# Kernel tuning notes

Hardware: AMD Instinct MI355X
Metric: run time of the kernel (lower is better)

Reference implementation:

```python
import jax, jax.numpy as jnp
import numpy as np

MARGIN = 0.5
EPS = 1e-5
NOISE_RATE = 0.5


def setup_inputs() -> dict:
    key = jax.random.key(0)
    k1, k2, k3, k4, k5 = jax.random.split(key, 5)
    n, m, d, c = 1024, 65536, 512, 10000
    return {
        "inputs_col": jax.random.normal(k1, (n, d), dtype=jnp.float32),
        "inputs_row": jax.random.normal(k2, (m, d), dtype=jnp.float32),
        "center": jax.random.normal(k3, (c, d), dtype=jnp.float32),
        "targets_col": jax.random.randint(k4, (n,), 0, c, dtype=jnp.int64),
        "target_row": jax.random.randint(k5, (m,), 0, c, dtype=jnp.int64),
        "filled_mask": jnp.ones((c,), dtype=bool),
    }


def _prism_keep(features, targets, center, filled_mask, noise_rate):
    # no_grad in the original -> stop_gradient here
    f = jax.lax.stop_gradient(features)
    c = jax.lax.stop_gradient(center)
    # all_sim_exp[cls] / sum(all_sim_exp) is exactly softmax over class logits
    probs = jax.nn.softmax(f @ c.T, axis=-1)          # [n, num_classes]
    sel = jnp.take_along_axis(probs, targets[:, None], axis=1)[:, 0]  # [n]
    C = jnp.where(filled_mask[targets], sel, 1.0)      # not-in-memory -> 1
    n = C.shape[0]
    n_remove = int(noise_rate * n)                     # static
    to_remove = jnp.argsort(C)[:n_remove]
    # empty margin_window path: keep everything except to_remove
    keep = jnp.ones((n,), dtype=bool).at[to_remove].set(False)
    return keep


def reference(inputs_col, inputs_row, center, targets_col, target_row, filled_mask):
    n = inputs_col.shape[0]
    sim = inputs_col @ inputs_row.T                    # [n, m]
    pos_mask = targets_col[:, None] == target_row[None, :]
    neg_mask = (~pos_mask) & (sim > MARGIN)
    pos_mask = pos_mask & (sim < 1.0 - EPS)

    keep = _prism_keep(inputs_col, targets_col, center, filled_mask, NOISE_RATE)
    pos_mask = pos_mask & keep[:, None]
    neg_mask = neg_mask & keep[:, None]

    # sum over selected pairs without boolean-indexing (masked reductions)
    pos_loss = jnp.sum(jnp.where(pos_mask, 1.0 - sim, 0.0))
    neg_loss = jnp.sum(jnp.where(neg_mask, sim, 0.0))
    loss = (pos_loss + neg_loss) / n
    return loss, keep
```

## Files before the change

kernel.cpp:

```cpp
#include <hip/hip_runtime.h>


typedef int    v4i   __attribute__((ext_vector_type(4)));
typedef float  f32x4 __attribute__((ext_vector_type(4)));
typedef unsigned char u8;

#define N_COL  1024
#define M_ROW  65536
#define DDIM   512
#define NCLS   10000
#define NT     79
#define NREM   512

#define OFF_A8   0u
#define OFF_C8   524288u
#define OFF_PMS  39256064u
#define OFF_LT   39903232u
#define OFF_COMP 39907328u
#define OFF_TCC  39909376u
#define OFF_ACC  39911424u
#define OFF_CNT  39911432u

__device__ __forceinline__ void async16(const void* g, void* l) {
    __builtin_amdgcn_global_load_lds(
        (const __attribute__((address_space(1))) void*)g,
        (__attribute__((address_space(3))) void*)l, 16, 0, 0);
}

__device__ __forceinline__ unsigned pack4_fp8(float4 v) {
    int r = 0;
    r = __builtin_amdgcn_cvt_pk_fp8_f32(v.x, v.y, r, false);
    r = __builtin_amdgcn_cvt_pk_fp8_f32(v.z, v.w, r, true);
    return (unsigned)r;
}

__device__ __forceinline__ void gemm8_128(const u8* __restrict__ A,
                                          const u8* __restrict__ B,
                                          int m0, int n0,
                                          u8* As, u8* Bs, f32x4 (&acc)[4][4]) {
    const int tid = threadIdx.x, wid = tid >> 6, lane = tid & 63;
    const int wm = wid >> 1, wn = wid & 1;
    const int q = lane >> 4, lc = lane & 15;

    const u8* gA[4]; const u8* gB[4]; int voff[4];
#pragma unroll
    for (int s = 0; s < 4; ++s) {
        const int c  = wid * 256 + s * 64 + lane;
        const int r  = c >> 3;
        const int gs = (c & 7) ^ (r & 7);
        gA[s] = A + (size_t)(m0 + r) * DDIM + gs * 16;
        gB[s] = B + (size_t)(n0 + r) * DDIM + gs * 16;
        voff[s] = c * 16;
    }
#pragma unroll
    for (int i = 0; i < 4; ++i)
#pragma unroll
        for (int j = 0; j < 4; ++j) acc[i][j] = (f32x4){0.f, 0.f, 0.f, 0.f};

    for (int kt = 0; kt < 4; ++kt) {
        const int kb = kt * 128;
#pragma unroll
        for (int s = 0; s < 4; ++s) {
            async16(gA[s] + kb, As + voff[s]);
            async16(gB[s] + kb, Bs + voff[s]);
        }
        __syncthreads();
#pragma unroll
        for (int ks = 0; ks < 4; ++ks) {
            const int gg = ks * 2 + (q >> 1);
            const int bo = (q & 1) * 8;
            long long af[4], bv[4];
#pragma unroll
            for (int i = 0; i < 4; ++i) {
                const int rA = wm * 64 + i * 16 + lc;
                af[i] = *(const long long*)(As + (rA * 8 + (gg ^ (rA & 7))) * 16 + bo);
                const int rB = wn * 64 + i * 16 + lc;
                bv[i] = *(const long long*)(Bs + (rB * 8 + (gg ^ (rB & 7))) * 16 + bo);
            }
#pragma unroll
            for (int i = 0; i < 4; ++i)
#pragma unroll
                for (int j = 0; j < 4; ++j)
                    acc[i][j] = __builtin_amdgcn_mfma_f32_16x16x32_fp8_fp8(
                        af[i], bv[j], acc[i][j], 0, 0, 0);
        }
        __syncthreads();
    }
}

__global__ void k_prep(const float4* __restrict__ a4, const float4* __restrict__ c4,
                       const float* __restrict__ a32, const float* __restrict__ c32,
                       const int* __restrict__ tcol,
                       unsigned* __restrict__ A8w, uint2* __restrict__ C8w,
                       float* __restrict__ lt, double* __restrict__ accd,
                       unsigned* __restrict__ cnt) {
    const int b = blockIdx.x, tid = threadIdx.x;
    if (b == 0 && tid == 0) { *accd = 0.0; *cnt = 0u; }
    if (b < 256) {
        const int idx = b * 256 + tid;
        A8w[idx * 2]     = pack4_fp8(a4[idx * 2]);
        A8w[idx * 2 + 1] = pack4_fp8(a4[idx * 2 + 1]);
    } else if (b < 2784) {
        const int cidx = (b - 256) * 256 + tid;
        const int row  = cidx >> 6;
        uint2 o = make_uint2(0u, 0u);
        if (row < NCLS) {
            o.x = pack4_fp8(c4[cidx * 2]);
            o.y = pack4_fp8(c4[cidx * 2 + 1]);
        }
        C8w[cidx] = o;
    } else {
        const int w = (b - 2784) * 4 + (tid >> 6), lane = tid & 63;
        const int t = tcol[w];
        const float* ar = a32 + (size_t)w * DDIM;
        const float* cr = c32 + (size_t)t * DDIM;
        float s = 0.f;
#pragma unroll
        for (int k = 0; k < DDIM / 64; ++k) s += ar[lane + k * 64] * cr[lane + k * 64];
        for (int off = 32; off; off >>= 1) s += __shfl_down(s, off, 64);
        if (lane == 0) lt[w] = s;
    }
}

__global__ __launch_bounds__(256, 3) void k_mid(const u8* __restrict__ A8,
                                                const u8* __restrict__ C8,
                                                float2* __restrict__ pms) {
    const int b = blockIdx.x, tid = threadIdx.x;
    __shared__ __align__(16) u8 As[16384], Bs[16384];
    __shared__ float s_mm[128][2], s_ss[128][2];
    const int n_t = b >> 3, m0 = (b & 7) * 128, n0 = n_t * 128;
    f32x4 acc[4][4];
    gemm8_128(A8, C8, m0, n0, As, Bs, acc);

    const int wid = tid >> 6, lane = tid & 63;
    const int wm = wid >> 1, wn = wid & 1, q = lane >> 4, lc = lane & 15;
    const int cbase = n0 + wn * 64 + lc;
#pragma unroll
    for (int i = 0; i < 4; ++i) {
#pragma unroll
        for (int reg = 0; reg < 4; ++reg) {
            float mm = -INFINITY, ss = 0.f;
#pragma unroll
            for (int j = 0; j < 4; ++j)
                if (cbase + j * 16 < NCLS) mm = fmaxf(mm, acc[i][j][reg]);
#pragma unroll
            for (int j = 0; j < 4; ++j)
                if (cbase + j * 16 < NCLS) ss += __expf(acc[i][j][reg] - mm);
#pragma unroll
            for (int d2 = 1; d2 < 16; d2 <<= 1) {
                float mo = __shfl_xor(mm, d2, 16);
                float so = __shfl_xor(ss, d2, 16);
                float M = fmaxf(mm, mo), S = 0.f;
                if (ss > 0.f) S += ss * __expf(mm - M);
                if (so > 0.f) S += so * __expf(mo - M);
                mm = M; ss = S;
            }
            if (lc == 0) {
                const int row = i * 16 + q * 4 + reg;
                s_mm[wm * 64 + row][wn] = mm;
                s_ss[wm * 64 + row][wn] = ss;
            }
        }
    }
    __syncthreads();
    if (tid < 128) {
        float m1 = s_mm[tid][0], s1 = s_ss[tid][0];
        float m2 = s_mm[tid][1], s2 = s_ss[tid][1];
        float M = fmaxf(m1, m2), S = 0.f;
        if (s1 > 0.f) S += s1 * __expf(m1 - M);
        if (s2 > 0.f) S += s2 * __expf(m2 - M);
        pms[(size_t)n_t * N_COL + m0 + tid] = make_float2(M, S);
    }
}

__global__ __launch_bounds__(1024) void k_sel(const float2* __restrict__ pms,
                                              const float* __restrict__ lt,
                                              const int* __restrict__ tcol,
                                              int* __restrict__ comp,
                                              int* __restrict__ tcc,
                                              float* __restrict__ keep_out) {
    __shared__ float v[N_COL];
    const int i = threadIdx.x;
    float M = -INFINITY, S = 0.f;
    for (int t = 0; t < NT; ++t) {
        float2 p = pms[(size_t)t * N_COL + i];
        if (p.y > 0.f) {
            if (p.x > M) { S = S * __expf(M - p.x) + p.y; M = p.x; }
            else         { S += p.y * __expf(p.x - M); }
        }
    }
    const float x = lt[i] - (M + logf(S));
    v[i] = x;
    __syncthreads();
    int rank = 0;
    const float4* v4 = (const float4*)v;
#pragma unroll 8
    for (int j4 = 0; j4 < N_COL / 4; ++j4) {
        float4 w = v4[j4];
        const int j = j4 * 4;
        rank += (w.x < x) || (w.x == x && j     < i);
        rank += (w.y < x) || (w.y == x && j + 1 < i);
        rank += (w.z < x) || (w.z == x && j + 2 < i);
        rank += (w.w < x) || (w.w == x && j + 3 < i);
    }
    const bool keep = rank >= NREM;
    keep_out[i] = keep ? 1.0f : 0.0f;
    if (keep) { comp[rank - NREM] = i; tcc[rank - NREM] = tcol[i]; }
}

__global__ __launch_bounds__(512, 2) void k_loss(const u8* __restrict__ A8,
                                                 const float4* __restrict__ brow4,
                                                 const int* __restrict__ comp,
                                                 const int* __restrict__ tcc,
                                                 const int* __restrict__ trow,
                                                 double* __restrict__ accd,
                                                 unsigned* __restrict__ cnt,
                                                 float* __restrict__ out) {
    __shared__ __align__(16) u8 As[3][32768];
    __shared__ __align__(16) u8 Bs[2][8192];
    __shared__ int s_map[512], s_tc[512], s_tr[128];
    __shared__ float s_red[8];
    const int b = blockIdx.x, tid = threadIdx.x;
    const int n0 = b * 128;
    s_map[tid] = comp[tid];
    s_tc[tid]  = tcc[tid];
    if (tid < 128) s_tr[tid] = trow[n0 + tid];
    __syncthreads();

    const int wid = tid >> 6, lane = tid & 63;
    const int wm = wid >> 1, wn = wid & 1;
    const int q = lane >> 4, lc = lane & 15;

    const u8* gA[4]; int vA[4];
#pragma unroll
    for (int s = 0; s < 4; ++s) {
        const int cc = s * 512 + tid;
        const int r  = cc >> 2, gpos = cc & 3;
        const int g  = gpos ^ ((r >> 1) & 3);
        gA[s] = A8 + (size_t)s_map[r] * DDIM + g * 16;
        vA[s] = cc * 16;
    }
    const int rB0 = tid >> 2, gB0 = tid & 3;
    const float4* gB = brow4 + (size_t)(n0 + rB0) * (DDIM / 4) + gB0 * 4;
    const int vB = (rB0 * 4 + (gB0 ^ ((rB0 >> 1) & 3))) * 16;

    f32x4 acc[8][4];
#pragma unroll
    for (int i = 0; i < 8; ++i)
#pragma unroll
        for (int j = 0; j < 4; ++j) acc[i][j] = (f32x4){0.f, 0.f, 0.f, 0.f};

    auto compute = [&](const u8* Asc, const u8* Bsc) {
#pragma unroll
        for (int ks = 0; ks < 2; ++ks) {
            const int gg = ks * 2 + (q >> 1);
            const int bo = (q & 1) * 8;
            long long af[8], bv[4];
#pragma unroll
            for (int i = 0; i < 8; ++i) {
                const int rA = wm * 128 + i * 16 + lc;
                af[i] = *(const long long*)(Asc + (rA * 4 + (gg ^ ((rA >> 1) & 3))) * 16 + bo);
            }
#pragma unroll
            for (int j = 0; j < 4; ++j) {
                const int rB = wn * 64 + j * 16 + lc;
                bv[j] = *(const long long*)(Bsc + (rB * 4 + (gg ^ ((rB >> 1) & 3))) * 16 + bo);
            }
#pragma unroll
            for (int i = 0; i < 8; ++i)
#pragma unroll
                for (int j = 0; j < 4; ++j)
                    acc[i][j] = __builtin_amdgcn_mfma_f32_16x16x32_fp8_fp8(
                        af[i], bv[j], acc[i][j], 0, 0, 0);
        }
    };

    float4 fb[2][4];

#pragma unroll
    for (int s = 0; s < 4; ++s) async16(gA[s], As[0] + vA[s]);
#pragma unroll
    for (int g = 0; g < 4; ++g) fb[0][g] = gB[g];
    __builtin_amdgcn_sched_barrier(0);
#pragma unroll
    for (int s = 0; s < 4; ++s) async16(gA[s] + 64, As[1] + vA[s]);
#pragma unroll
    for (int g = 0; g < 4; ++g) fb[1][g] = gB[16 + g];
    asm volatile("s_waitcnt vmcnt(8)" ::: "memory");
    __builtin_amdgcn_sched_barrier(0);
    {
        uint4 pk;
        pk.x = pack4_fp8(fb[0][0]); pk.y = pack4_fp8(fb[0][1]);
        pk.z = pack4_fp8(fb[0][2]); pk.w = pack4_fp8(fb[0][3]);
        *(uint4*)(Bs[0] + vB) = pk;
    }
    asm volatile("s_waitcnt lgkmcnt(0)" ::: "memory");
    __builtin_amdgcn_s_barrier();

#pragma unroll
    for (int kt = 0; kt < 8; ++kt) {
        if (kt < 6) {
            const int kb = (kt + 2) * 64;
#pragma unroll
            for (int s = 0; s < 4; ++s) async16(gA[s] + kb, As[(kt + 2) % 3] + vA[s]);
#pragma unroll
            for (int g = 0; g < 4; ++g) fb[kt & 1][g] = gB[(kt + 2) * 16 + g];
            asm volatile("s_waitcnt vmcnt(8)" ::: "memory");
        } else if (kt == 6) {
            asm volatile("s_waitcnt vmcnt(0)" ::: "memory");
        }
        __builtin_amdgcn_sched_barrier(0);
        if (kt < 7) {
            uint4 pk;
            pk.x = pack4_fp8(fb[(kt + 1) & 1][0]); pk.y = pack4_fp8(fb[(kt + 1) & 1][1]);
            pk.z = pack4_fp8(fb[(kt + 1) & 1][2]); pk.w = pack4_fp8(fb[(kt + 1) & 1][3]);
            *(uint4*)(Bs[(kt + 1) & 1] + vB) = pk;
        }
        compute(As[kt % 3], Bs[kt & 1]);
        if (kt < 7) {
            asm volatile("s_waitcnt lgkmcnt(0)" ::: "memory");
            __builtin_amdgcn_s_barrier();
        }
    }

    const float POSMAX = 1.0f - 1e-5f;
    float local = 0.f;
#pragma unroll
    for (int i = 0; i < 8; ++i) {
#pragma unroll
        for (int j = 0; j < 4; ++j) {
            const int tr = s_tr[wn * 64 + j * 16 + lc];
#pragma unroll
            for (int reg = 0; reg < 4; ++reg) {
                const int row = wm * 128 + i * 16 + q * 4 + reg;
                const float sim = acc[i][j][reg];
                if (s_tc[row] == tr) {
                    if (sim < POSMAX) local += 1.0f - sim;
                } else if (sim > 0.5f) {
                    local += sim;
                }
            }
        }
    }
    for (int off = 32; off; off >>= 1) local += __shfl_down(local, off, 64);
    if (lane == 0) s_red[wid] = local;
    __syncthreads();
    if (tid == 0) {
        float blk = 0.f;
#pragma unroll
        for (int w = 0; w < 8; ++w) blk += s_red[w];
        atomicAdd(accd, (double)blk);
        __threadfence();
        if (atomicAdd(cnt, 1u) == 511u) {
            double vfin = atomicAdd(accd, 0.0);
            out[0] = (float)(vfin / (double)N_COL);
        }
    }
}

extern "C" void kernel_launch(void* const* d_in, const int* in_sizes, int n_in,
                              void* d_out, int out_size, void* d_ws, size_t ws_size,
                              hipStream_t stream) {
    (void)in_sizes; (void)n_in; (void)out_size; (void)ws_size;
    const float* inputs_col  = (const float*)d_in[0];
    const float* inputs_row  = (const float*)d_in[1];
    const float* center      = (const float*)d_in[2];
    const int*   targets_col = (const int*)d_in[3];
    const int*   target_row  = (const int*)d_in[4];
    float* out = (float*)d_out;
    char*  ws  = (char*)d_ws;

    u8*       A8   = (u8*)(ws + OFF_A8);
    u8*       C8   = (u8*)(ws + OFF_C8);
    float2*   pms  = (float2*)(ws + OFF_PMS);
    float*    lt   = (float*) (ws + OFF_LT);
    int*      comp = (int*)   (ws + OFF_COMP);
    int*      tcc  = (int*)   (ws + OFF_TCC);
    double*   accd = (double*)(ws + OFF_ACC);
    unsigned* cnt  = (unsigned*)(ws + OFF_CNT);

    k_prep<<<3040, 256, 0, stream>>>((const float4*)inputs_col, (const float4*)center,
                                     inputs_col, center, targets_col,
                                     (unsigned*)A8, (uint2*)C8, lt, accd, cnt);
    k_mid<<<632, 256, 0, stream>>>(A8, C8, pms);
    k_sel<<<1, 1024, 0, stream>>>(pms, lt, targets_col, comp, tcc, out + 1);
    k_loss<<<512, 512, 0, stream>>>(A8, (const float4*)inputs_row,
                                    comp, tcc, target_row, accd, cnt, out);
}
```

Baseline: 337.3 us.

## Split selection kernel across blocks and interleave loss GEMM loads with MFMA phases

The single-block selection kernel becomes two 16-block kernels: one computes the per-row log-sum-exp, the other ranks the rows, so the work is spread over more compute units. The k_loss main loop is broken into four sub-phases per k-tile. Each phase interleaves LDS fragment reads and staggered global prefetches with MFMA bursts, adds s_setprio around the MFMAs, and places extra barriers between phases. This aims to hide load latency behind matrix math, but it adds barriers and one more kernel launch.

```diff
diff --git a/kernel.cpp b/kernel.cpp
--- a/kernel.cpp
+++ b/kernel.cpp
@@ -18,8 +18,9 @@
 #define OFF_LT   39903232u
 #define OFF_COMP 39907328u
 #define OFF_TCC  39909376u
-#define OFF_ACC  39911424u
-#define OFF_CNT  39911432u
+#define OFF_LOGC 39911424u
+#define OFF_ACC  39915520u
+#define OFF_CNT  39915528u
 
 __device__ __forceinline__ void async16(const void* g, void* l) {
     __builtin_amdgcn_global_load_lds(
@@ -173,14 +174,10 @@
     }
 }
 
-__global__ __launch_bounds__(1024) void k_sel(const float2* __restrict__ pms,
-                                              const float* __restrict__ lt,
-                                              const int* __restrict__ tcol,
-                                              int* __restrict__ comp,
-                                              int* __restrict__ tcc,
-                                              float* __restrict__ keep_out) {
-    __shared__ float v[N_COL];
-    const int i = threadIdx.x;
+__global__ void k_lse(const float2* __restrict__ pms,
+                      const float* __restrict__ lt,
+                      float* __restrict__ logc) {
+    const int i = blockIdx.x * 64 + threadIdx.x;
     float M = -INFINITY, S = 0.f;
     for (int t = 0; t < NT; ++t) {
         float2 p = pms[(size_t)t * N_COL + i];
@@ -189,9 +186,23 @@
             else         { S += p.y * __expf(p.x - M); }
         }
     }
-    const float x = lt[i] - (M + logf(S));
-    v[i] = x;
+    logc[i] = lt[i] - (M + logf(S));
+}
+
+__global__ __launch_bounds__(64) void k_rank(const float* __restrict__ logc,
+                                             const int* __restrict__ tcol,
+                                             int* __restrict__ comp,
+                                             int* __restrict__ tcc,
+                                             float* __restrict__ keep_out) {
+    __shared__ float v[N_COL];
+    const int t = threadIdx.x, b = blockIdx.x;
+    const float4* g4 = (const float4*)logc;
+    float4* vs = (float4*)v;
+#pragma unroll
+    for (int s = 0; s < 4; ++s) vs[t + s * 64] = g4[t + s * 64];
     __syncthreads();
+    const int i = b * 64 + t;
+    const float x = v[i];
     int rank = 0;
     const float4* v4 = (const float4*)v;
 #pragma unroll 8
@@ -250,31 +261,6 @@
 #pragma unroll
         for (int j = 0; j < 4; ++j) acc[i][j] = (f32x4){0.f, 0.f, 0.f, 0.f};
 
-    auto compute = [&](const u8* Asc, const u8* Bsc) {
-#pragma unroll
-        for (int ks = 0; ks < 2; ++ks) {
-            const int gg = ks * 2 + (q >> 1);
-            const int bo = (q & 1) * 8;
-            long long af[8], bv[4];
-#pragma unroll
-            for (int i = 0; i < 8; ++i) {
-                const int rA = wm * 128 + i * 16 + lc;
-                af[i] = *(const long long*)(Asc + (rA * 4 + (gg ^ ((rA >> 1) & 3))) * 16 + bo);
-            }
-#pragma unroll
-            for (int j = 0; j < 4; ++j) {
-                const int rB = wn * 64 + j * 16 + lc;
-                bv[j] = *(const long long*)(Bsc + (rB * 4 + (gg ^ ((rB >> 1) & 3))) * 16 + bo);
-            }
-#pragma unroll
-            for (int i = 0; i < 8; ++i)
-#pragma unroll
-                for (int j = 0; j < 4; ++j)
-                    acc[i][j] = __builtin_amdgcn_mfma_f32_16x16x32_fp8_fp8(
-                        af[i], bv[j], acc[i][j], 0, 0, 0);
-        }
-    };
-
     float4 fb[2][4];
 
 #pragma unroll
@@ -295,31 +281,129 @@
         *(uint4*)(Bs[0] + vB) = pk;
     }
     asm volatile("s_waitcnt lgkmcnt(0)" ::: "memory");
+    __builtin_amdgcn_sched_barrier(0);
     __builtin_amdgcn_s_barrier();
 
 #pragma unroll
     for (int kt = 0; kt < 8; ++kt) {
-        if (kt < 6) {
-            const int kb = (kt + 2) * 64;
-#pragma unroll
-            for (int s = 0; s < 4; ++s) async16(gA[s] + kb, As[(kt + 2) % 3] + vA[s]);
-#pragma unroll
-            for (int g = 0; g < 4; ++g) fb[kt & 1][g] = gB[(kt + 2) * 16 + g];
-            asm volatile("s_waitcnt vmcnt(8)" ::: "memory");
-        } else if (kt == 6) {
-            asm volatile("s_waitcnt vmcnt(0)" ::: "memory");
-        }
-        __builtin_amdgcn_sched_barrier(0);
-        if (kt < 7) {
-            uint4 pk;
-            pk.x = pack4_fp8(fb[(kt + 1) & 1][0]); pk.y = pack4_fp8(fb[(kt + 1) & 1][1]);
-            pk.z = pack4_fp8(fb[(kt + 1) & 1][2]); pk.w = pack4_fp8(fb[(kt + 1) & 1][3]);
-            *(uint4*)(Bs[(kt + 1) & 1] + vB) = pk;
-        }
-        compute(As[kt % 3], Bs[kt & 1]);
-        if (kt < 7) {
+        const u8* Asc = As[kt % 3];
+        const u8* Bsc = Bs[kt & 1];
+        const int kb2 = (kt + 2) * 64;
+        const int s2  = (kt + 2) % 3;
+        const int bo  = (q & 1) * 8;
+        long long af[4], bv[4];
+
+        {
+            const int gg = (q >> 1);
+#pragma unroll
+            for (int i = 0; i < 4; ++i) {
+                const int rA = wm * 128 + i * 16 + lc;
+                af[i] = *(const long long*)(Asc + (rA * 4 + (gg ^ ((rA >> 1) & 3))) * 16 + bo);
+            }
+#pragma unroll
+            for (int j = 0; j < 4; ++j) {
+                const int rB = wn * 64 + j * 16 + lc;
+                bv[j] = *(const long long*)(Bsc + (rB * 4 + (gg ^ ((rB >> 1) & 3))) * 16 + bo);
+            }
+            if (kt < 6) { async16(gA[0] + kb2, As[s2] + vA[0]);
+                          async16(gA[1] + kb2, As[s2] + vA[1]); }
+            __builtin_amdgcn_s_barrier();
             asm volatile("s_waitcnt lgkmcnt(0)" ::: "memory");
-            __builtin_amdgcn_s_barrier();
+            __builtin_amdgcn_sched_barrier(0);
+            __builtin_amdgcn_s_setprio(1);
+#pragma unroll
+            for (int i = 0; i < 4; ++i)
+#pragma unroll
+                for (int j = 0; j < 4; ++j)
+                    acc[i][j] = __builtin_amdgcn_mfma_f32_16x16x32_fp8_fp8(
+                        af[i], bv[j], acc[i][j], 0, 0, 0);
+            __builtin_amdgcn_s_setprio(0);
+            __builtin_amdgcn_s_barrier();
+        }
+        {
+            const int gg = (q >> 1);
+            long long a2[4];
+#pragma unroll
+            for (int i = 0; i < 4; ++i) {
+                const int rA = wm * 128 + (4 + i) * 16 + lc;
+                a2[i] = *(const long long*)(Asc + (rA * 4 + (gg ^ ((rA >> 1) & 3))) * 16 + bo);
+            }
+            if (kt < 6) { async16(gA[2] + kb2, As[s2] + vA[2]);
+                          async16(gA[3] + kb2, As[s2] + vA[3]); }
+            __builtin_amdgcn_s_barrier();
+            asm volatile("s_waitcnt lgkmcnt(0)" ::: "memory");
+            __builtin_amdgcn_sched_barrier(0);
+            __builtin_amdgcn_s_setprio(1);
+#pragma unroll
+            for (int i = 0; i < 4; ++i)
+#pragma unroll
+                for (int j = 0; j < 4; ++j)
+                    acc[4 + i][j] = __builtin_amdgcn_mfma_f32_16x16x32_fp8_fp8(
+                        a2[i], bv[j], acc[4 + i][j], 0, 0, 0);
+            __builtin_amdgcn_s_setprio(0);
+            __builtin_amdgcn_s_barrier();
+        }
+        {
+            const int gg = 2 + (q >> 1);
+#pragma unroll
+            for (int i = 0; i < 4; ++i) {
+                const int rA = wm * 128 + i * 16 + lc;
+                af[i] = *(const long long*)(Asc + (rA * 4 + (gg ^ ((rA >> 1) & 3))) * 16 + bo);
+            }
+#pragma unroll
+            for (int j = 0; j < 4; ++j) {
+                const int rB = wn * 64 + j * 16 + lc;
+                bv[j] = *(const long long*)(Bsc + (rB * 4 + (gg ^ ((rB >> 1) & 3))) * 16 + bo);
+            }
+            if (kt < 6) {
+#pragma unroll
+                for (int g = 0; g < 4; ++g) fb[kt & 1][g] = gB[(kt + 2) * 16 + g];
+            }
+            __builtin_amdgcn_s_barrier();
+            asm volatile("s_waitcnt lgkmcnt(0)" ::: "memory");
+            __builtin_amdgcn_sched_barrier(0);
+            __builtin_amdgcn_s_setprio(1);
+#pragma unroll
+            for (int i = 0; i < 4; ++i)
+#pragma unroll
+                for (int j = 0; j < 4; ++j)
+                    acc[i][j] = __builtin_amdgcn_mfma_f32_16x16x32_fp8_fp8(
+                        af[i], bv[j], acc[i][j], 0, 0, 0);
+            __builtin_amdgcn_s_setprio(0);
+            __builtin_amdgcn_s_barrier();
+        }
+        {
+            const int gg = 2 + (q >> 1);
+            long long a2[4];
+#pragma unroll
+            for (int i = 0; i < 4; ++i) {
+                const int rA = wm * 128 + (4 + i) * 16 + lc;
+                a2[i] = *(const long long*)(Asc + (rA * 4 + (gg ^ ((rA >> 1) & 3))) * 16 + bo);
+            }
+            if (kt < 7) {
+                uint4 pk;
+                pk.x = pack4_fp8(fb[(kt + 1) & 1][0]); pk.y = pack4_fp8(fb[(kt + 1) & 1][1]);
+                pk.z = pack4_fp8(fb[(kt + 1) & 1][2]); pk.w = pack4_fp8(fb[(kt + 1) & 1][3]);
+                *(uint4*)(Bs[(kt + 1) & 1] + vB) = pk;
+            }
+            if (kt < 6) {
+                asm volatile("s_waitcnt vmcnt(8)" ::: "memory");
+            } else if (kt == 6) {
+                asm volatile("s_waitcnt vmcnt(0)" ::: "memory");
+            }
+            __builtin_amdgcn_sched_barrier(0);
+            __builtin_amdgcn_s_barrier();
+            asm volatile("s_waitcnt lgkmcnt(0)" ::: "memory");
+            __builtin_amdgcn_sched_barrier(0);
+            __builtin_amdgcn_s_setprio(1);
+#pragma unroll
+            for (int i = 0; i < 4; ++i)
+#pragma unroll
+                for (int j = 0; j < 4; ++j)
+                    acc[4 + i][j] = __builtin_amdgcn_mfma_f32_16x16x32_fp8_fp8(
+                        a2[i], bv[j], acc[4 + i][j], 0, 0, 0);
+            __builtin_amdgcn_s_setprio(0);
+            if (kt < 7) __builtin_amdgcn_s_barrier();
         }
     }
 
@@ -376,6 +460,7 @@
     float*    lt   = (float*) (ws + OFF_LT);
     int*      comp = (int*)   (ws + OFF_COMP);
     int*      tcc  = (int*)   (ws + OFF_TCC);
+    float*    logc = (float*) (ws + OFF_LOGC);
     double*   accd = (double*)(ws + OFF_ACC);
     unsigned* cnt  = (unsigned*)(ws + OFF_CNT);
 
@@ -383,7 +468,8 @@
                                      inputs_col, center, targets_col,
                                      (unsigned*)A8, (uint2*)C8, lt, accd, cnt);
     k_mid<<<632, 256, 0, stream>>>(A8, C8, pms);
-    k_sel<<<1, 1024, 0, stream>>>(pms, lt, targets_col, comp, tcc, out + 1);
+    k_lse<<<16, 64, 0, stream>>>(pms, lt, logc);
+    k_rank<<<16, 64, 0, stream>>>(logc, targets_col, comp, tcc, out + 1);
     k_loss<<<512, 512, 0, stream>>>(A8, (const float4*)inputs_row,
                                     comp, tcc, target_row, accd, cnt, out);
 }
```

After: 321.9 us. -4.6%, faster.
